# Optimization experiments

Measured on AMD Instinct MI355X. Metric: run time of the kernel, lower is better.

The kernel has to match this reference:

```python
import jax, jax.numpy as jnp
import numpy as np

HID = 512      # out_channels / HR2O hidden_dim
CIN = 2048     # conv1 input channels (Cf + Cx)
DEPTH = 3
EPS = 1e-5     # GroupNorm eps


def conv2d(x, w, pad):
    return jax.lax.conv_general_dilated(
        x, w, window_strides=(1, 1), padding=[(pad, pad), (pad, pad)],
        dimension_numbers=('NCHW', 'OIHW', 'NCHW'))


def hr2o(x, wq, wk, wv, wm, gamma, beta):
    # x: [N, C, H, W]
    q = conv2d(x, wq, 1)
    k = conv2d(x, wk, 1)
    v = conv2d(x, wv, 1)
    # (query.unsqueeze(1) * key.unsqueeze(0)).sum(2) / sqrt(C) -> [N, N, H, W]
    att = jnp.einsum('qchw,kchw->qkhw', q, k) / jnp.sqrt(jnp.float32(HID))
    att = jax.nn.softmax(att, axis=1)  # softmax over key dim
    # (att.unsqueeze(2) * value).sum(1) -> [N, C, H, W]
    vf = jnp.einsum('qkhw,kchw->qchw', att, v)
    # GroupNorm(1, C): normalize over (C, H, W), per-channel affine
    mu = jnp.mean(vf, axis=(1, 2, 3), keepdims=True)
    var = jnp.var(vf, axis=(1, 2, 3), keepdims=True)
    vf = (vf - mu) * jax.lax.rsqrt(var + EPS)
    vf = vf * gamma[None, :, None, None] + beta[None, :, None, None]
    vf = jax.nn.relu(vf)
    vf = conv2d(vf, wm, 1)
    # Dropout(0.2) is identity in eval mode
    return x + vf


def setup_inputs() -> dict:
    key = jax.random.key(0)
    ks = jax.random.split(key, 12)
    N, B = 32, 8
    Cx, Cf, H, W = 1024, 1024, 16, 16
    s = 0.02
    return {
        'x': jax.random.normal(ks[0], (N, Cx, 4, 7, 7), jnp.float32),
        'feat': jax.random.normal(ks[1], (B, Cf, 1, H, W), jnp.float32),
        'rois': jax.random.randint(ks[2], (N, 5), 0, B, jnp.int32),
        'w1': jax.random.normal(ks[3], (HID, CIN, 1, 1), jnp.float32) * s,
        'w2': jax.random.normal(ks[4], (HID, HID, 3, 3), jnp.float32) * s,
        'wq': jax.random.normal(ks[5], (DEPTH, HID, HID, 3, 3), jnp.float32) * s,
        'wk': jax.random.normal(ks[6], (DEPTH, HID, HID, 3, 3), jnp.float32) * s,
        'wv': jax.random.normal(ks[7], (DEPTH, HID, HID, 3, 3), jnp.float32) * s,
        'wm': jax.random.normal(ks[8], (DEPTH, HID, HID, 3, 3), jnp.float32) * s,
        'gamma': jnp.ones((DEPTH, HID), jnp.float32),
        'beta': jnp.zeros((DEPTH, HID), jnp.float32),
    }


def reference(x, feat, rois, w1, w2, wq, wk, wv, wm, gamma, beta):
    n, cx = x.shape[0], x.shape[1]
    # AdaptiveMaxPool3d(1) -> [N, Cx, 1, 1, 1]
    xp = jnp.max(x, axis=(2, 3, 4), keepdims=True)
    h, w = feat.shape[-2], feat.shape[-1]
    roi_inds = rois[:, 0].astype(jnp.int32)
    roi_gfeat = feat[roi_inds]                              # [N, Cf, 1, H, W]
    x_tile = jnp.broadcast_to(xp, (n, cx, 1, h, w))         # repeat(1,1,1,h,w)
    nf = jnp.concatenate([roi_gfeat, x_tile], axis=1)[:, :, 0]  # squeeze(2)
    nf = jax.nn.relu(conv2d(nf, w1, 0))                     # 1x1 conv
    nf = jax.nn.relu(conv2d(nf, w2, 0))                     # 3x3 conv, no pad
    for i in range(DEPTH):
        nf = hr2o(nf, wq[i], wk[i], wv[i], wm[i], gamma[i], beta[i])
    nf = jnp.mean(nf, axis=(2, 3), keepdims=True)[:, :, None]  # gap -> [N,C,1,1,1]
    return jnp.concatenate([xp, nf], axis=1)                # [N, Cx+HID, 1, 1, 1]
```

## Files before the change

kernel.cpp:

```cpp
#include <hip/hip_runtime.h>


typedef __attribute__((ext_vector_type(8))) short bhalf8;
typedef __attribute__((ext_vector_type(4))) float floatx4;

#define ACT_N 131072
#define W3SZ  2359296

__device__ inline float b2f(unsigned short u) {
  union { unsigned int i; float f; } x; x.i = ((unsigned int)u) << 16; return x.f;
}
__device__ inline unsigned short f2b(float f) {
  union { float f; unsigned int i; } x; x.f = f;
  return (unsigned short)((x.i + 0x7FFFu + ((x.i >> 16) & 1u)) >> 16);
}
__device__ inline void gload_lds16(const unsigned short* g, bhalf8* l) {
  __builtin_amdgcn_global_load_lds(
      (const __attribute__((address_space(1))) unsigned int*)(const void*)g,
      (__attribute__((address_space(3))) unsigned int*)(void*)l, 16, 0, 0);
}
template <int N> __device__ inline void waitvm() {
  asm volatile("s_waitcnt vmcnt(%0)" :: "i"(N) : "memory");
}
__device__ inline void phase_barrier_pre() {
  __builtin_amdgcn_sched_barrier(0);
  __builtin_amdgcn_s_barrier();
  __builtin_amdgcn_sched_barrier(0);
}
__device__ inline void phase_barrier_post() {
  __builtin_amdgcn_sched_barrier(0);
  __builtin_amdgcn_s_barrier();
  __builtin_amdgcn_sched_barrier(0);
}

__global__ void pool_max_kernel(const float* __restrict__ x, float* __restrict__ xp,
                                float* __restrict__ out) {
  int tid = threadIdx.x;
  int wid = blockIdx.x * 4 + (tid >> 6);
  int lane = tid & 63;
  int n = wid >> 10, c = wid & 1023;
  const float* p = x + (size_t)wid * 196;
  float v = -3.4e38f;
  v = fmaxf(v, p[lane]);
  v = fmaxf(v, p[lane + 64]);
  v = fmaxf(v, p[lane + 128]);
  if (lane < 4) v = fmaxf(v, p[lane + 192]);
#pragma unroll
  for (int off = 32; off >= 1; off >>= 1) v = fmaxf(v, __shfl_xor(v, off));
  if (lane == 0) { xp[wid] = v; out[(size_t)n * 1536 + c] = v; }
}

__global__ void bias1_kernel(const float* __restrict__ w1, const float* __restrict__ xp,
                             float* __restrict__ bias1) {
  int tid = threadIdx.x;
  int wid = blockIdx.x * 4 + (tid >> 6);
  int lane = tid & 63;
  int n = wid >> 9, o = wid & 511;
  const float* wr = w1 + (size_t)o * 2048 + 1024;
  const float* xr = xp + (size_t)n * 1024;
  float s = 0.f;
#pragma unroll
  for (int r = 0; r < 16; r++) { int c = lane + r * 64; s += wr[c] * xr[c]; }
#pragma unroll
  for (int off = 32; off >= 1; off >>= 1) s += __shfl_xor(s, off);
  if (lane == 0) bias1[wid] = s;
}

__global__ __launch_bounds__(256) void wprep3_kernel(
    const float* __restrict__ w2, const float* __restrict__ wq,
    const float* __restrict__ wk, const float* __restrict__ wv,
    const float* __restrict__ wm, unsigned short* __restrict__ Wg2) {
  int ks = blockIdx.x, ot = blockIdx.y, tid = blockIdx.z;
  int t = threadIdx.x;
  const float* src;
  if (tid == 0) src = w2;
  else {
    int d = (tid - 1) >> 2, r = (tid - 1) & 3;
    src = (r == 0 ? wq : r == 1 ? wk : r == 2 ? wv : wm) + (size_t)d * W3SZ;
  }
  __shared__ unsigned short S[64 * 288];
  const float* sb = src + (size_t)ot * 64 * 4608 + (size_t)ks * 288;
  for (int j = 0; j < 72; j++) {
    int flat = j * 256 + t;
    int o = flat / 288, ci = flat % 288;
    S[flat] = f2b(sb[(size_t)o * 4608 + ci]);
  }
  __syncthreads();
  unsigned short* dst = Wg2 + (((size_t)(tid * 8 + ot) * 16 + ks) * 2304) * 8;
#pragma unroll
  for (int s = 0; s < 9; s++) {
    int u = t + s * 256;
    int g = u / 768, rem = u % 768;
    int rl = rem >> 6, o = rem & 63;
    int dh = rl >> 2, kg = rl & 3;
    int t9src = dh * 3 + g;
    bhalf8 v;
#pragma unroll
    for (int j = 0; j < 8; j++) v[j] = (short)S[o * 288 + (kg * 8 + j) * 9 + t9src];
    *(bhalf8*)(dst + (size_t)u * 8) = v;
  }
}

__global__ void w1prep_kernel(const float* __restrict__ w1, unsigned short* __restrict__ W1g) {
  int ks = blockIdx.x, ot = blockIdx.y, t = threadIdx.x;
  int kg = t >> 6, o = t & 63;
  const float* s = w1 + (size_t)(ot * 64 + o) * 2048 + ks * 32 + kg * 8;
  bhalf8 v;
#pragma unroll
  for (int j = 0; j < 8; j++) v[j] = (short)f2b(s[j]);
  *(bhalf8*)(W1g + (((size_t)ot * 32 + ks) * 256 + t) * 8) = v;
}

__global__ __launch_bounds__(256) void ftprep_kernel(
    const float* __restrict__ feat, unsigned short* __restrict__ featT) {
  int img = blockIdx.z, c0 = blockIdx.y * 64, p0 = blockIdx.x * 64;
  int t = threadIdx.x;
  int a = t >> 6, b = t & 63;
  __shared__ float S[64][65];
#pragma unroll
  for (int j = 0; j < 16; j++) {
    int r = a * 16 + j;
    S[r][b] = feat[((size_t)img * 1024 + c0 + r) * 256 + p0 + b];
  }
  __syncthreads();
#pragma unroll
  for (int j = 0; j < 16; j++) {
    int pl = a * 16 + j;
    featT[((size_t)img * 256 + p0 + pl) * 1024 + c0 + b] = f2b(S[b][pl]);
  }
}

template <int TAPS, int KTOT, int WAVES, int NREP, int PSPLIT,
          bool RELU, bool ADD, bool BIAS, bool VALID>
__global__ __launch_bounds__(WAVES * 64) void conv_mfma_kernel(
    const unsigned short* __restrict__ Xg, const int* __restrict__ rois,
    const unsigned short* __restrict__ Wg, const float* __restrict__ bias,
    unsigned short* __restrict__ Out) {
  constexpr int THREADS = WAVES * 64;
  constexpr int NK = KTOT / 32;
  static_assert(PSPLIT * WAVES * NREP * 16 == 256, "p coverage");

  int n = blockIdx.x;
  int ot = blockIdx.y / PSPLIT;
  int pq = blockIdx.y % PSPLIT;
  int t = threadIdx.x;
  int wv = t >> 6, l = t & 63, l15 = l & 15, l4 = l >> 4;
  int pbase = (pq * WAVES + wv) * (NREP * 16);
  const unsigned short* xb =
      Xg + (rois ? (size_t)rois[n * 5] * 256 * KTOT : (size_t)n * 256 * KTOT);
  floatx4 acc[4][NREP] = {};

  if constexpr (TAPS == 9) {
    constexpr int LW = 768 / THREADS;
    constexpr int LX = 1024 / THREADS;
    static_assert(768 % THREADS == 0 && 1024 % THREADS == 0, "stage div");
    __shared__ bhalf8 Xs[2][1024];
    __shared__ bhalf8 Wl[3][768];

    auto stageX = [&](int xbuf, int ks) {
#pragma unroll
      for (int i = 0; i < LX; i++) {
        int base = i * THREADS + wv * 64;
        int u = base + l;
        int p = u & 255, kg = u >> 8;
        gload_lds16(xb + (size_t)p * KTOT + ks * 32 + kg * 8, &Xs[xbuf][base]);
      }
    };
    auto stageW = [&](int wbuf, int ks, int g) {
      const unsigned short* wb =
          Wg + (((size_t)ot * NK + ks) * 2304 + g * 768) * 8;
#pragma unroll
      for (int i = 0; i < LW; i++) {
        int base = i * THREADS + wv * 64;
        gload_lds16(wb + (size_t)(base + l) * 8, &Wl[wbuf][base]);
      }
    };
    auto computeG = [&](const bhalf8* X, const bhalf8* W, int g) {
      bhalf8 BW[NREP + 2];
#pragma unroll
      for (int w10 = 0; w10 < NREP + 2; w10++) {
        int row = (pbase + w10 * 16 + l15 + g) & 255;
        BW[w10] = X[l4 * 256 + row];
      }
      bhalf8 A[3][4];
#pragma unroll
      for (int dh = 0; dh < 3; dh++)
#pragma unroll
        for (int of = 0; of < 4; of++)
          A[dh][of] = W[(dh * 4 + l4) * 64 + of * 16 + l15];
      __builtin_amdgcn_s_setprio(1);
#pragma unroll
      for (int dh = 0; dh < 3; dh++)
#pragma unroll
        for (int of = 0; of < 4; of++)
#pragma unroll
          for (int pf = 0; pf < NREP; pf++)
            acc[of][pf] = __builtin_amdgcn_mfma_f32_16x16x32_bf16(
                A[dh][of], BW[pf + dh], acc[of][pf], 0, 0, 0);
      __builtin_amdgcn_s_setprio(0);
    };

    stageW(0, 0, 0); stageX(0, 0);
    stageW(1, 0, 1);

    for (int ks = 0; ks < NK - 1; ks++) {
      const bhalf8* X = Xs[ks & 1];
      stageW(2, ks, 2);
      waitvm<2 * LW>();
      phase_barrier_pre();
      computeG(X, Wl[0], 0);
      phase_barrier_post();
      stageW(0, ks + 1, 0); stageX((ks + 1) & 1, ks + 1);
      waitvm<2 * LW + LX>();
      phase_barrier_pre();
      computeG(X, Wl[1], 1);
      phase_barrier_post();
      stageW(1, ks + 1, 1);
      waitvm<2 * LW + LX>();
      phase_barrier_pre();
      computeG(X, Wl[2], 2);
      phase_barrier_post();
    }
    {
      const bhalf8* X = Xs[(NK - 1) & 1];
      stageW(2, NK - 1, 2);
      waitvm<2 * LW>();
      phase_barrier_pre();
      computeG(X, Wl[0], 0);
      phase_barrier_post();
      waitvm<LW>();
      phase_barrier_pre();
      computeG(X, Wl[1], 1);
      phase_barrier_post();
      waitvm<0>();
      phase_barrier_pre();
      computeG(X, Wl[2], 2);
      phase_barrier_post();
    }
  } else {
    constexpr int LW = 256 / THREADS;
    constexpr int LX = 1024 / THREADS;
    static_assert(256 % THREADS == 0 && 1024 % THREADS == 0, "stage div");
    __shared__ bhalf8 Xs[3][1024];
    __shared__ bhalf8 Wl[3][256];

    auto stage1 = [&](int b, int ks) {
#pragma unroll
      for (int i = 0; i < LX; i++) {
        int base = i * THREADS + wv * 64;
        int u = base + l;
        int p = u & 255, kg = u >> 8;
        gload_lds16(xb + (size_t)p * KTOT + ks * 32 + kg * 8, &Xs[b][base]);
      }
      const unsigned short* wb = Wg + (((size_t)ot * NK + ks) * 256) * 8;
#pragma unroll
      for (int i = 0; i < LW; i++) {
        int base = i * THREADS + wv * 64;
        gload_lds16(wb + (size_t)(base + l) * 8, &Wl[b][base]);
      }
    };
    auto compute1 = [&](const bhalf8* X, const bhalf8* W) {
      bhalf8 B[NREP];
#pragma unroll
      for (int pf = 0; pf < NREP; pf++) {
        int row = (pbase + pf * 16 + l15) & 255;
        B[pf] = X[l4 * 256 + row];
      }
      bhalf8 A[4];
#pragma unroll
      for (int of = 0; of < 4; of++) A[of] = W[l4 * 64 + of * 16 + l15];
      __builtin_amdgcn_s_setprio(1);
#pragma unroll
      for (int of = 0; of < 4; of++)
#pragma unroll
        for (int pf = 0; pf < NREP; pf++)
          acc[of][pf] = __builtin_amdgcn_mfma_f32_16x16x32_bf16(
              A[of], B[pf], acc[of][pf], 0, 0, 0);
      __builtin_amdgcn_s_setprio(0);
    };

    stage1(0, 0);
    stage1(1, 1);
    int b = 0;
    for (int ks = 0; ks < NK - 2; ks++) {
      int b2 = b + 2; if (b2 >= 3) b2 -= 3;
      stage1(b2, ks + 2);
      waitvm<2 * (LW + LX)>();
      phase_barrier_pre();
      compute1(Xs[b], Wl[b]);
      phase_barrier_post();
      b = b + 1; if (b >= 3) b -= 3;
    }
    waitvm<LW + LX>();
    phase_barrier_pre();
    compute1(Xs[b], Wl[b]);
    phase_barrier_post();
    b = b + 1; if (b >= 3) b -= 3;
    waitvm<0>();
    phase_barrier_pre();
    compute1(Xs[b], Wl[b]);
    phase_barrier_post();
  }

#pragma unroll
  for (int of = 0; of < 4; of++) {
    int og = ot * 64 + of * 16 + l4 * 4;
    int tensor = og >> 9, ol = og & 511;
#pragma unroll
    for (int pf = 0; pf < NREP; pf++) {
      int p = pbase + pf * 16 + l15;
      int po = p;
      if (VALID) {
        int h = p >> 4, w = p & 15;
        if (h >= 14 || w >= 14) continue;
        po = (h + 1) * 16 + (w + 1);
      }
      unsigned short* dp = Out + (((size_t)tensor * 32 + n) * 256 + po) * 512 + ol;
      float vv[4];
#pragma unroll
      for (int r2 = 0; r2 < 4; r2++) vv[r2] = acc[of][pf][r2];
      if (BIAS) {
#pragma unroll
        for (int r2 = 0; r2 < 4; r2++) vv[r2] += bias[(size_t)n * 512 + ol + r2];
      }
      if (ADD) {
        ushort4 old = *(const ushort4*)dp;
        vv[0] += b2f(old.x); vv[1] += b2f(old.y); vv[2] += b2f(old.z); vv[3] += b2f(old.w);
      }
      if (RELU) {
#pragma unroll
        for (int r2 = 0; r2 < 4; r2++) vv[r2] = fmaxf(vv[r2], 0.f);
      }
      ushort4 st = { f2b(vv[0]), f2b(vv[1]), f2b(vv[2]), f2b(vv[3]) };
      *(ushort4*)dp = st;
    }
  }
}

__global__ __launch_bounds__(256) void vtrans_kernel(
    const unsigned short* __restrict__ v, unsigned short* __restrict__ vt) {
  int ppc = blockIdx.x;
  int pp = (ppc / 14 + 1) * 16 + ppc % 14 + 1;
  int t = threadIdx.x;
  __shared__ unsigned short S[32 * 512];
#pragma unroll
  for (int i = 0; i < 8; i++) {
    int u = i * 256 + t;
    int kn = u >> 6, c8 = (u & 63) * 8;
    *(bhalf8*)&S[kn * 512 + c8] = *(const bhalf8*)(v + ((size_t)kn * 256 + pp) * 512 + c8);
  }
  __syncthreads();
#pragma unroll
  for (int half = 0; half < 2; half++) {
    int c = half * 256 + t;
    unsigned int col[16];
#pragma unroll
    for (int j = 0; j < 16; j++)
      col[j] = (unsigned int)S[(2 * j) * 512 + c] |
               ((unsigned int)S[(2 * j + 1) * 512 + c] << 16);
    unsigned short* dst = vt + ((size_t)ppc * 512 + c) * 32;
#pragma unroll
    for (int j = 0; j < 4; j++) {
      uint4 P = { col[j * 4], col[j * 4 + 1], col[j * 4 + 2], col[j * 4 + 3] };
      *(uint4*)(dst + j * 8) = P;
    }
  }
}

__global__ __launch_bounds__(64) void attfused_kernel(
    const unsigned short* __restrict__ q, const unsigned short* __restrict__ k,
    const unsigned short* __restrict__ vt, unsigned short* __restrict__ out,
    float* __restrict__ gnpart) {
  int pp = blockIdx.x;
  int h = pp >> 4, w = pp & 15;
  int l = threadIdx.x, l15 = l & 15, l4 = l >> 4;
  if (h < 1 || h > 14 || w < 1 || w > 14) {
    uint4 z = {0u, 0u, 0u, 0u};
#pragma unroll
    for (int qn = 0; qn < 32; qn++)
      *(uint4*)(out + ((size_t)qn * 256 + pp) * 512 + l * 8) = z;
    return;
  }
  int ppc = (h - 1) * 14 + (w - 1);

  floatx4 sc[2][2] = {};
#pragma unroll
  for (int kb = 0; kb < 16; kb++) {
    bhalf8 A[2], B[2];
#pragma unroll
    for (int of = 0; of < 2; of++)
      A[of] = *(const bhalf8*)(k + ((size_t)(of * 16 + l15) * 256 + pp) * 512 + kb * 32 + l4 * 8);
#pragma unroll
    for (int pf = 0; pf < 2; pf++)
      B[pf] = *(const bhalf8*)(q + ((size_t)(pf * 16 + l15) * 256 + pp) * 512 + kb * 32 + l4 * 8);
#pragma unroll
    for (int of = 0; of < 2; of++)
#pragma unroll
      for (int pf = 0; pf < 2; pf++)
        sc[of][pf] = __builtin_amdgcn_mfma_f32_16x16x32_bf16(A[of], B[pf], sc[of][pf], 0, 0, 0);
  }

  __shared__ unsigned short p_lds[32 * 32];
  const float scale = 0.044194173824159216f;
#pragma unroll
  for (int pf = 0; pf < 2; pf++) {
    float v8[8];
    float m = -3.4e38f;
#pragma unroll
    for (int of = 0; of < 2; of++)
#pragma unroll
      for (int r = 0; r < 4; r++) {
        float x = sc[of][pf][r] * scale;
        v8[of * 4 + r] = x;
        m = fmaxf(m, x);
      }
    m = fmaxf(m, __shfl_xor(m, 16));
    m = fmaxf(m, __shfl_xor(m, 32));
    float s = 0.f;
#pragma unroll
    for (int i = 0; i < 8; i++) { v8[i] = __expf(v8[i] - m); s += v8[i]; }
    s += __shfl_xor(s, 16);
    s += __shfl_xor(s, 32);
    float inv = 1.f / s;
#pragma unroll
    for (int of = 0; of < 2; of++) {
      ushort4 pk = { f2b(v8[of * 4 + 0] * inv), f2b(v8[of * 4 + 1] * inv),
                     f2b(v8[of * 4 + 2] * inv), f2b(v8[of * 4 + 3] * inv) };
      *(ushort4*)&p_lds[(pf * 16 + l15) * 32 + of * 16 + l4 * 4] = pk;
    }
  }

  bhalf8 PB[2];
#pragma unroll
  for (int qf = 0; qf < 2; qf++)
    PB[qf] = *(const bhalf8*)&p_lds[(qf * 16 + l15) * 32 + l4 * 8];
  float gs[2] = {0.f, 0.f}, gss[2] = {0.f, 0.f};
  const unsigned short* vtb = vt + (size_t)ppc * 512 * 32;
#pragma unroll
  for (int chunk = 0; chunk < 4; chunk++) {
    bhalf8 VA[8];
#pragma unroll
    for (int co = 0; co < 8; co++)
      VA[co] = *(const bhalf8*)(vtb + (size_t)(chunk * 128 + co * 16 + l15) * 32 + l4 * 8);
#pragma unroll
    for (int co = 0; co < 8; co++)
#pragma unroll
      for (int qf = 0; qf < 2; qf++) {
        floatx4 pa = __builtin_amdgcn_mfma_f32_16x16x32_bf16(
            VA[co], PB[qf], (floatx4){0.f, 0.f, 0.f, 0.f}, 0, 0, 0);
        float x0 = pa[0], x1 = pa[1], x2 = pa[2], x3 = pa[3];
        gs[qf] += x0 + x1 + x2 + x3;
        gss[qf] += x0 * x0 + x1 * x1 + x2 * x2 + x3 * x3;
        ushort4 st = { f2b(x0), f2b(x1), f2b(x2), f2b(x3) };
        int qn = qf * 16 + l15;
        int c = chunk * 128 + co * 16 + l4 * 4;
        *(ushort4*)(out + ((size_t)qn * 256 + pp) * 512 + c) = st;
      }
  }
#pragma unroll
  for (int qf = 0; qf < 2; qf++) {
    gs[qf] += __shfl_xor(gs[qf], 16);  gs[qf] += __shfl_xor(gs[qf], 32);
    gss[qf] += __shfl_xor(gss[qf], 16); gss[qf] += __shfl_xor(gss[qf], 32);
  }
  if (l4 == 0) {
#pragma unroll
    for (int qf = 0; qf < 2; qf++) {
      int qn = qf * 16 + l15;
      gnpart[((size_t)ppc * 32 + qn) * 2]     = gs[qf];
      gnpart[((size_t)ppc * 32 + qn) * 2 + 1] = gss[qf];
    }
  }
}

__global__ __launch_bounds__(256) void gnapply3_kernel(
    unsigned short* __restrict__ x, const float* __restrict__ gnpart,
    const float* __restrict__ gamma, const float* __restrict__ beta) {
  int n = blockIdx.y, half = blockIdx.x, t = threadIdx.x;
  float s = 0.f, ss = 0.f;
  if (t < 196) {
    s  = gnpart[((size_t)t * 32 + n) * 2];
    ss = gnpart[((size_t)t * 32 + n) * 2 + 1];
  }
#pragma unroll
  for (int off = 32; off >= 1; off >>= 1) { s += __shfl_xor(s, off); ss += __shfl_xor(ss, off); }
  __shared__ float sm[8];
  int wv = t >> 6, ln = t & 63;
  if (ln == 0) { sm[wv] = s; sm[4 + wv] = ss; }
  __syncthreads();
  float S = sm[0] + sm[1] + sm[2] + sm[3];
  float SS = sm[4] + sm[5] + sm[6] + sm[7];
  const float M = 512.f * 196.f;
  float mu = S / M;
  float var = SS / M - mu * mu;
  float inv = rsqrtf(var + 1e-5f);
  int c2 = t * 2;
  unsigned short* xb = x + (size_t)n * ACT_N;
  float g0 = gamma[c2], g1 = gamma[c2 + 1];
  float be0 = beta[c2], be1 = beta[c2 + 1];
  for (int i = 0; i < 98; i++) {
    int ppc = half * 98 + i;
    int pp = (ppc / 14 + 1) * 16 + ppc % 14 + 1;
    unsigned int vv = *(unsigned int*)(xb + pp * 512 + c2);
    float a = (b2f((unsigned short)vv) - mu) * inv * g0 + be0;
    float b = (b2f((unsigned short)(vv >> 16)) - mu) * inv * g1 + be1;
    a = fmaxf(a, 0.f); b = fmaxf(b, 0.f);
    *(unsigned int*)(xb + pp * 512 + c2) =
        (unsigned int)f2b(a) | ((unsigned int)f2b(b) << 16);
  }
}

__global__ void fmean2_kernel(const unsigned short* __restrict__ x, float* __restrict__ out) {
  int n = blockIdx.x, t = threadIdx.x;
  const unsigned short* xb = x + (size_t)n * ACT_N;
  float s0 = 0.f, s1 = 0.f;
  for (int i = 0; i < 196; i++) {
    int pp = (i / 14 + 1) * 16 + (i % 14) + 1;
    unsigned int vv = *(const unsigned int*)(xb + pp * 512 + t * 2);
    s0 += b2f((unsigned short)vv);
    s1 += b2f((unsigned short)(vv >> 16));
  }
  out[(size_t)n * 1536 + 1024 + t * 2]     = s0 * (1.f / 196.f);
  out[(size_t)n * 1536 + 1024 + t * 2 + 1] = s1 * (1.f / 196.f);
}

extern "C" void kernel_launch(void* const* d_in, const int* in_sizes, int n_in,
                              void* d_out, int out_size, void* d_ws, size_t ws_size,
                              hipStream_t stream) {
  const float* x     = (const float*)d_in[0];
  const float* feat  = (const float*)d_in[1];
  const int*   rois  = (const int*)d_in[2];
  const float* w1    = (const float*)d_in[3];
  const float* w2    = (const float*)d_in[4];
  const float* wq    = (const float*)d_in[5];
  const float* wk    = (const float*)d_in[6];
  const float* wv    = (const float*)d_in[7];
  const float* wm    = (const float*)d_in[8];
  const float* gamma = (const float*)d_in[9];
  const float* beta  = (const float*)d_in[10];
  float* out = (float*)d_out;

  float* wsf   = (float*)d_ws;
  float* xp    = wsf;
  float* bias1 = xp + 32768;
  float* stats = bias1 + 16384;
  float* attf  = stats + 64;
  unsigned short* ub    = (unsigned short*)(attf + 262144);
  unsigned short* featT = ub;
  unsigned short* W1g   = featT + 2097152;
  unsigned short* Wg2   = W1g + 524288;
  unsigned short* bufq  = Wg2 + 30670848;
  unsigned short* bufk  = bufq + 4194304;
  unsigned short* bufv  = bufk + 4194304;
  unsigned short* bufx  = bufv + 4194304;
  unsigned short* vt    = (unsigned short*)d_ws;
  float* gnpart = (float*)(bufx + 4194304);

  hipMemsetAsync(bufx, 0, (size_t)4194304 * 2, stream);

  pool_max_kernel<<<8192, 256, 0, stream>>>(x, xp, out);
  bias1_kernel<<<4096, 256, 0, stream>>>(w1, xp, bias1);
  wprep3_kernel<<<dim3(16, 8, 13), 256, 0, stream>>>(w2, wq, wk, wv, wm, Wg2);
  w1prep_kernel<<<dim3(32, 8), 256, 0, stream>>>(w1, W1g);
  ftprep_kernel<<<dim3(4, 16, 8), 256, 0, stream>>>(feat, featT);

  conv_mfma_kernel<1, 1024, 4, 4, 1, true, false, true, false>
      <<<dim3(32, 8), 256, 0, stream>>>(featT, rois, W1g, bias1, bufq);
  conv_mfma_kernel<9, 512, 4, 4, 1, true, false, false, true>
      <<<dim3(32, 8), 256, 0, stream>>>(bufq, nullptr, Wg2, nullptr, bufx);

  for (int d = 0; d < 3; d++) {
    conv_mfma_kernel<9, 512, 4, 4, 1, false, false, false, true>
        <<<dim3(32, 24), 256, 0, stream>>>(bufx, nullptr,
            Wg2 + (size_t)(1 + 4 * d) * W3SZ, nullptr, bufq);
    vtrans_kernel<<<196, 256, 0, stream>>>(bufv, vt);
    attfused_kernel<<<256, 64, 0, stream>>>(bufq, bufk, vt, bufq, gnpart);
    gnapply3_kernel<<<dim3(2, 32), 256, 0, stream>>>(bufq, gnpart,
        gamma + d * 512, beta + d * 512);
    conv_mfma_kernel<9, 512, 4, 4, 1, false, true, false, true>
        <<<dim3(32, 8), 256, 0, stream>>>(bufq, nullptr,
            Wg2 + (size_t)(4 + 4 * d) * W3SZ, nullptr, bufx);
  }

  fmean2_kernel<<<32, 256, 0, stream>>>(bufx, out);
}
```

Measured before the change: 766.7 us.

## Software-pipeline conv MFMA loop with register double-buffering and single barrier per phase

Restructures the main loops of both conv kernels so LDS-to-register fragment loads for the next phase are issued before the current phase's MFMAs, using two register sets that alternate. Each phase now ends with one vmcnt(0) wait and one barrier instead of two barriers with partial waits. It also adds a min-blocks-per-CU hint of 2 to launch bounds. The aim is to hide LDS read latency behind MFMA work and cut synchronization, but it doubles fragment registers and waits for all outstanding global loads each phase.

```diff
diff --git a/kernel.cpp b/kernel.cpp
--- a/kernel.cpp
+++ b/kernel.cpp
@@ -22,15 +22,11 @@
 template <int N> __device__ inline void waitvm() {
   asm volatile("s_waitcnt vmcnt(%0)" :: "i"(N) : "memory");
 }
-__device__ inline void phase_barrier_pre() {
-  __builtin_amdgcn_sched_barrier(0);
+__device__ inline void SB() { __builtin_amdgcn_sched_barrier(0); }
+__device__ inline void endphase() {
+  SB(); waitvm<0>();
   __builtin_amdgcn_s_barrier();
-  __builtin_amdgcn_sched_barrier(0);
-}
-__device__ inline void phase_barrier_post() {
-  __builtin_amdgcn_sched_barrier(0);
-  __builtin_amdgcn_s_barrier();
-  __builtin_amdgcn_sched_barrier(0);
+  SB();
 }
 
 __global__ void pool_max_kernel(const float* __restrict__ x, float* __restrict__ xp,
@@ -132,13 +128,14 @@
 
 template <int TAPS, int KTOT, int WAVES, int NREP, int PSPLIT,
           bool RELU, bool ADD, bool BIAS, bool VALID>
-__global__ __launch_bounds__(WAVES * 64) void conv_mfma_kernel(
+__global__ __launch_bounds__(WAVES * 64, 2) void conv_mfma_kernel(
     const unsigned short* __restrict__ Xg, const int* __restrict__ rois,
     const unsigned short* __restrict__ Wg, const float* __restrict__ bias,
     unsigned short* __restrict__ Out) {
   constexpr int THREADS = WAVES * 64;
   constexpr int NK = KTOT / 32;
   static_assert(PSPLIT * WAVES * NREP * 16 == 256, "p coverage");
+  static_assert((NK & 1) == 0, "even NK");
 
   int n = blockIdx.x;
   int ot = blockIdx.y / PSPLIT;
@@ -151,7 +148,6 @@
   floatx4 acc[4][NREP] = {};
 
   if constexpr (TAPS == 9) {
-    constexpr int LW = 768 / THREADS;
     constexpr int LX = 1024 / THREADS;
     static_assert(768 % THREADS == 0 && 1024 % THREADS == 0, "stage div");
     __shared__ bhalf8 Xs[2][1024];
@@ -170,24 +166,24 @@
       const unsigned short* wb =
           Wg + (((size_t)ot * NK + ks) * 2304 + g * 768) * 8;
 #pragma unroll
-      for (int i = 0; i < LW; i++) {
+      for (int i = 0; i < 768 / THREADS; i++) {
         int base = i * THREADS + wv * 64;
         gload_lds16(wb + (size_t)(base + l) * 8, &Wl[wbuf][base]);
       }
     };
-    auto computeG = [&](const bhalf8* X, const bhalf8* W, int g) {
-      bhalf8 BW[NREP + 2];
-#pragma unroll
-      for (int w10 = 0; w10 < NREP + 2; w10++) {
-        int row = (pbase + w10 * 16 + l15 + g) & 255;
-        BW[w10] = X[l4 * 256 + row];
-      }
-      bhalf8 A[3][4];
+    auto ldregs = [&](bhalf8 (&BW)[NREP + 2], bhalf8 (&A)[12], int ks, int g) {
+      const bhalf8* X = Xs[ks & 1];
+#pragma unroll
+      for (int w10 = 0; w10 < NREP + 2; w10++)
+        BW[w10] = X[l4 * 256 + ((pbase + w10 * 16 + l15 + g) & 255)];
+      const bhalf8* W = Wl[g];
 #pragma unroll
       for (int dh = 0; dh < 3; dh++)
 #pragma unroll
         for (int of = 0; of < 4; of++)
-          A[dh][of] = W[(dh * 4 + l4) * 64 + of * 16 + l15];
+          A[dh * 4 + of] = W[(dh * 4 + l4) * 64 + of * 16 + l15];
+    };
+    auto domfma = [&](bhalf8 (&BW)[NREP + 2], bhalf8 (&A)[12]) {
       __builtin_amdgcn_s_setprio(1);
 #pragma unroll
       for (int dh = 0; dh < 3; dh++)
@@ -196,49 +192,44 @@
 #pragma unroll
           for (int pf = 0; pf < NREP; pf++)
             acc[of][pf] = __builtin_amdgcn_mfma_f32_16x16x32_bf16(
-                A[dh][of], BW[pf + dh], acc[of][pf], 0, 0, 0);
+                A[dh * 4 + of], BW[pf + dh], acc[of][pf], 0, 0, 0);
       __builtin_amdgcn_s_setprio(0);
     };
 
-    stageW(0, 0, 0); stageX(0, 0);
-    stageW(1, 0, 1);
-
-    for (int ks = 0; ks < NK - 1; ks++) {
-      const bhalf8* X = Xs[ks & 1];
-      stageW(2, ks, 2);
-      waitvm<2 * LW>();
-      phase_barrier_pre();
-      computeG(X, Wl[0], 0);
-      phase_barrier_post();
-      stageW(0, ks + 1, 0); stageX((ks + 1) & 1, ks + 1);
-      waitvm<2 * LW + LX>();
-      phase_barrier_pre();
-      computeG(X, Wl[1], 1);
-      phase_barrier_post();
+    bhalf8 BW0[NREP + 2], A0[12], BW1[NREP + 2], A1[12];
+
+    stageX(0, 0); stageW(0, 0, 0);
+    endphase();
+    ldregs(BW0, A0, 0, 0); SB();
+    stageW(1, 0, 1); stageX(1, 1);
+    endphase();
+
+    for (int ks = 0; ks < NK; ks += 2) {
+      ldregs(BW1, A1, ks, 1); SB();
+      stageW(2, ks, 2); SB();
+      domfma(BW0, A0); endphase();
+      ldregs(BW0, A0, ks, 2); SB();
+      stageW(0, ks + 1, 0); SB();
+      domfma(BW1, A1); endphase();
+      ldregs(BW1, A1, ks + 1, 0); SB();
       stageW(1, ks + 1, 1);
-      waitvm<2 * LW + LX>();
-      phase_barrier_pre();
-      computeG(X, Wl[2], 2);
-      phase_barrier_post();
-    }
-    {
-      const bhalf8* X = Xs[(NK - 1) & 1];
-      stageW(2, NK - 1, 2);
-      waitvm<2 * LW>();
-      phase_barrier_pre();
-      computeG(X, Wl[0], 0);
-      phase_barrier_post();
-      waitvm<LW>();
-      phase_barrier_pre();
-      computeG(X, Wl[1], 1);
-      phase_barrier_post();
-      waitvm<0>();
-      phase_barrier_pre();
-      computeG(X, Wl[2], 2);
-      phase_barrier_post();
+      if (ks + 2 < NK) stageX(ks & 1, ks + 2);
+      SB();
+      domfma(BW0, A0); endphase();
+      ldregs(BW0, A0, ks + 1, 1); SB();
+      stageW(2, ks + 1, 2); SB();
+      domfma(BW1, A1); endphase();
+      ldregs(BW1, A1, ks + 1, 2); SB();
+      if (ks + 2 < NK) stageW(0, ks + 2, 0);
+      SB();
+      domfma(BW0, A0); endphase();
+      if (ks + 2 < NK) { ldregs(BW0, A0, ks + 2, 0); SB(); }
+      if (ks + 2 < NK) stageW(1, ks + 2, 1);
+      if (ks + 3 < NK) stageX((ks + 1) & 1, ks + 3);
+      SB();
+      domfma(BW1, A1); endphase();
     }
   } else {
-    constexpr int LW = 256 / THREADS;
     constexpr int LX = 1024 / THREADS;
     static_assert(256 % THREADS == 0 && 1024 % THREADS == 0, "stage div");
     __shared__ bhalf8 Xs[3][1024];
@@ -254,21 +245,21 @@
       }
       const unsigned short* wb = Wg + (((size_t)ot * NK + ks) * 256) * 8;
 #pragma unroll
-      for (int i = 0; i < LW; i++) {
+      for (int i = 0; i < 256 / THREADS; i++) {
         int base = i * THREADS + wv * 64;
         gload_lds16(wb + (size_t)(base + l) * 8, &Wl[b][base]);
       }
     };
-    auto compute1 = [&](const bhalf8* X, const bhalf8* W) {
-      bhalf8 B[NREP];
-#pragma unroll
-      for (int pf = 0; pf < NREP; pf++) {
-        int row = (pbase + pf * 16 + l15) & 255;
-        B[pf] = X[l4 * 256 + row];
-      }
-      bhalf8 A[4];
+    auto ldregs1 = [&](bhalf8 (&B)[NREP], bhalf8 (&A)[4], int ks) {
+      const bhalf8* X = Xs[ks % 3];
+#pragma unroll
+      for (int pf = 0; pf < NREP; pf++)
+        B[pf] = X[l4 * 256 + ((pbase + pf * 16 + l15) & 255)];
+      const bhalf8* W = Wl[ks % 3];
 #pragma unroll
       for (int of = 0; of < 4; of++) A[of] = W[l4 * 64 + of * 16 + l15];
+    };
+    auto domfma1 = [&](bhalf8 (&B)[NREP], bhalf8 (&A)[4]) {
       __builtin_amdgcn_s_setprio(1);
 #pragma unroll
       for (int of = 0; of < 4; of++)
@@ -279,27 +270,22 @@
       __builtin_amdgcn_s_setprio(0);
     };
 
+    bhalf8 B0[NREP], A0[4], B1[NREP], A1[4];
     stage1(0, 0);
+    endphase();
+    ldregs1(B0, A0, 0); SB();
     stage1(1, 1);
-    int b = 0;
-    for (int ks = 0; ks < NK - 2; ks++) {
-      int b2 = b + 2; if (b2 >= 3) b2 -= 3;
-      stage1(b2, ks + 2);
-      waitvm<2 * (LW + LX)>();
-      phase_barrier_pre();
-      compute1(Xs[b], Wl[b]);
-      phase_barrier_post();
-      b = b + 1; if (b >= 3) b -= 3;
+    endphase();
+    for (int ks = 0; ks < NK; ks += 2) {
+      ldregs1(B1, A1, ks + 1); SB();
+      if (ks + 2 < NK) stage1((ks + 2) % 3, ks + 2);
+      SB();
+      domfma1(B0, A0); endphase();
+      if (ks + 2 < NK) { ldregs1(B0, A0, ks + 2); SB(); }
+      if (ks + 3 < NK) stage1((ks + 3) % 3, ks + 3);
+      SB();
+      domfma1(B1, A1); endphase();
     }
-    waitvm<LW + LX>();
-    phase_barrier_pre();
-    compute1(Xs[b], Wl[b]);
-    phase_barrier_post();
-    b = b + 1; if (b >= 3) b -= 3;
-    waitvm<0>();
-    phase_barrier_pre();
-    compute1(Xs[b], Wl[b]);
-    phase_barrier_post();
   }
 
 #pragma unroll
```

Result: faster. 681.5 us, median of 3 (-11.1%).
